# Kernel tuning notes

Measured on AMD Instinct MI355X. Metric: run time of the kernel, lower is better.

The kernel has to match this reference:

```python
import jax, jax.numpy as jnp
import numpy as np

HIDDEN = 2048
N_HEADS = 32
N_KV_HEADS = 4
HEAD_DIM = 128
EPS = 1e-6
ROPE_THETA = 1000000.0
B, S = 1, 2048


def setup_inputs() -> dict:
    key = jax.random.key(0)
    ks = jax.random.split(key, 7)
    scale = 0.02
    return {
        "hidden_states": jax.random.normal(ks[0], (B, S, HIDDEN), jnp.float32),
        "wq": jax.random.normal(ks[1], (HIDDEN, N_HEADS * HEAD_DIM), jnp.float32) * scale,
        "wk": jax.random.normal(ks[2], (HIDDEN, N_KV_HEADS * HEAD_DIM), jnp.float32) * scale,
        "wv": jax.random.normal(ks[3], (HIDDEN, N_KV_HEADS * HEAD_DIM), jnp.float32) * scale,
        "wo": jax.random.normal(ks[4], (N_HEADS * HEAD_DIM, HIDDEN), jnp.float32) * scale,
        "q_norm_w": jnp.ones((HEAD_DIM,), jnp.float32),
        "k_norm_w": jnp.ones((HEAD_DIM,), jnp.float32),
    }


def _rmsnorm(x, w, eps=EPS):
    # RMSNorm over last (head_dim) axis, as in Qwen3MoeRMSNorm applied per-head
    var = jnp.mean(jnp.square(x), axis=-1, keepdims=True)
    return x * jax.lax.rsqrt(var + eps) * w


def _rope_cos_sin(seq_len, dtype):
    inv_freq = 1.0 / (ROPE_THETA ** (jnp.arange(0, HEAD_DIM, 2, dtype=jnp.float32) / HEAD_DIM))
    pos = jnp.arange(seq_len, dtype=jnp.float32)
    freqs = pos[:, None] * inv_freq[None, :]          # [S, dh/2]
    emb = jnp.concatenate([freqs, freqs], axis=-1)    # [S, dh]
    return jnp.cos(emb).astype(dtype), jnp.sin(emb).astype(dtype)


def _rotate_half(x):
    h = x.shape[-1] // 2
    return jnp.concatenate([-x[..., h:], x[..., :h]], axis=-1)


def reference(hidden_states, wq, wk, wv, wo, q_norm_w, k_norm_w):
    b, s, _ = hidden_states.shape
    # QKV projections (bias-free)
    q = (hidden_states @ wq).reshape(b, s, N_HEADS, HEAD_DIM)
    k = (hidden_states @ wk).reshape(b, s, N_KV_HEADS, HEAD_DIM)
    v = (hidden_states @ wv).reshape(b, s, N_KV_HEADS, HEAD_DIM)
    # per-head RMSNorm on Q and K
    q = _rmsnorm(q, q_norm_w)
    k = _rmsnorm(k, k_norm_w)
    # RoPE (prefill, start_pos = 0)
    cos, sin = _rope_cos_sin(s, q.dtype)              # [S, dh]
    cos = cos[None, :, None, :]
    sin = sin[None, :, None, :]
    q = q * cos + _rotate_half(q) * sin
    k = k * cos + _rotate_half(k) * sin
    # GQA: repeat KV heads to match Q heads
    groups = N_HEADS // N_KV_HEADS
    k = jnp.repeat(k, groups, axis=2)                 # [B,S,nH,dh]
    v = jnp.repeat(v, groups, axis=2)
    # causal SDPA
    scaling = HEAD_DIM ** -0.5
    scores = jnp.einsum("bqhd,bkhd->bhqk", q, k) * scaling
    causal = jnp.tril(jnp.ones((s, s), dtype=bool))
    scores = jnp.where(causal[None, None], scores, jnp.finfo(scores.dtype).min)
    probs = jax.nn.softmax(scores, axis=-1)
    attn = jnp.einsum("bhqk,bkhd->bqhd", probs, v)    # [B,S,nH,dh]
    attn = attn.reshape(b, s, N_HEADS * HEAD_DIM)
    return attn @ wo
```

## Files before the change

### kernel.cpp

```cpp
#include <hip/hip_runtime.h>
#include <stdint.h>

typedef unsigned short u16;
typedef __bf16 bf16x8 __attribute__((ext_vector_type(8)));
typedef float f32x4 __attribute__((ext_vector_type(4)));

#define SEQ 2048
#define QKV_N 5120
#define QN 4096

#if __has_builtin(__builtin_amdgcn_exp2f)
#define EXP2F __builtin_amdgcn_exp2f
#else
#define EXP2F exp2f
#endif

#define QSC (0.08838834764831845f * 1.4426950408889634f)
#define MLOG2E 17.312340490667560f

__device__ __forceinline__ u16 f2bf(float f) {
  union { float f; unsigned u; } v; v.f = f;
  unsigned r = v.u + 0x7fffu + ((v.u >> 16) & 1u);
  return (u16)(r >> 16);
}
__device__ __forceinline__ u16 f2bf_fast(float f) {
  union { float f; unsigned u; } v; v.f = f;
  return (u16)((v.u + 0x8000u) >> 16);
}
__device__ __forceinline__ float bf2f(u16 b) {
  union { unsigned u; float f; } v; v.u = ((unsigned)b) << 16;
  return v.f;
}

__device__ __forceinline__ void gl2lds16(const void* g, void* l) {
  __builtin_amdgcn_global_load_lds((const __attribute__((address_space(1))) void*)g,
                                   (__attribute__((address_space(3))) void*)l, 16, 0, 0);
}

__global__ __launch_bounds__(256) void k_convert(const float* __restrict__ src, u16* __restrict__ dst) {
  int i = (blockIdx.x * 256 + threadIdx.x) * 4;
  float4 v = *(const float4*)(src + i);
  ushort4 o;
  o.x = f2bf(v.x); o.y = f2bf(v.y); o.z = f2bf(v.z); o.w = f2bf(v.w);
  *(ushort4*)(dst + i) = o;
}

__global__ __launch_bounds__(256) void k_transpose(const float* __restrict__ src, u16* __restrict__ dst,
                                                   int R, int C) {
  __shared__ float t[32][33];
  int c0 = blockIdx.x * 32, r0 = blockIdx.y * 32;
  int j = threadIdx.x & 31, i0 = threadIdx.x >> 5;
#pragma unroll
  for (int p = 0; p < 4; ++p) {
    int r = i0 + p * 8;
    t[r][j] = src[(size_t)(r0 + r) * C + c0 + j];
  }
  __syncthreads();
#pragma unroll
  for (int p = 0; p < 4; ++p) {
    int r = i0 + p * 8;
    dst[(size_t)(c0 + r) * R + r0 + j] = f2bf(t[j][r]);
  }
}

__global__ __launch_bounds__(256) void k_gemm160(const u16* __restrict__ A, const u16* __restrict__ BT,
                                                 u16* __restrict__ C, int M, int N, int K) {
  __shared__ u16 As[128 * 64];
  __shared__ u16 Bs[160 * 64];
  const int tid = threadIdx.x;
  const int w = tid >> 6, lane = tid & 63, quad = lane >> 4, l15 = lane & 15;
  const int m0 = blockIdx.y * 128, n0 = blockIdx.x * 160;
  const int mw = (w & 1) * 64, nw = (w >> 1) * 80;

  f32x4 acc[4][5];
#pragma unroll
  for (int i = 0; i < 4; ++i)
#pragma unroll
    for (int j = 0; j < 5; ++j) acc[i][j] = {0.f, 0.f, 0.f, 0.f};

  const int nk = K >> 6;
  for (int kt = 0; kt < nk; ++kt) {
    const int k0 = kt << 6;
    __syncthreads();
#pragma unroll
    for (int p = 0; p < 4; ++p) {
      int ci = (w * 4 + p) * 64 + lane;
      int row = ci >> 3, gc = (ci & 7) ^ (row & 7);
      gl2lds16(A + (size_t)(m0 + row) * K + k0 + gc * 8, As + (w * 4 + p) * 512);
    }
#pragma unroll
    for (int p = 0; p < 5; ++p) {
      int ci = (w * 5 + p) * 64 + lane;
      int row = ci >> 3, gc = (ci & 7) ^ (row & 7);
      gl2lds16(BT + (size_t)(n0 + row) * K + k0 + gc * 8, Bs + (w * 5 + p) * 512);
    }
    __syncthreads();
#pragma unroll
    for (int kk = 0; kk < 2; ++kk) {
      bf16x8 a[4], b[5];
#pragma unroll
      for (int mt = 0; mt < 4; ++mt) {
        int row = mw + mt * 16 + l15;
        a[mt] = *(const bf16x8*)(As + row * 64 + (((kk * 4 + quad) ^ (row & 7)) * 8));
      }
#pragma unroll
      for (int nt = 0; nt < 5; ++nt) {
        int row = nw + nt * 16 + l15;
        b[nt] = *(const bf16x8*)(Bs + row * 64 + (((kk * 4 + quad) ^ (row & 7)) * 8));
      }
#pragma unroll
      for (int mt = 0; mt < 4; ++mt)
#pragma unroll
        for (int nt = 0; nt < 5; ++nt)
          acc[mt][nt] = __builtin_amdgcn_mfma_f32_16x16x32_bf16(a[mt], b[nt], acc[mt][nt], 0, 0, 0);
    }
  }
#pragma unroll
  for (int mt = 0; mt < 4; ++mt)
#pragma unroll
    for (int nt = 0; nt < 5; ++nt)
#pragma unroll
      for (int r = 0; r < 4; ++r) {
        int row = m0 + mw + mt * 16 + quad * 4 + r;
        int col = n0 + nw + nt * 16 + l15;
        C[(size_t)row * N + col] = f2bf(acc[mt][nt][r]);
      }
}

__global__ __launch_bounds__(256) void k_gemm_sk(const u16* __restrict__ A, const u16* __restrict__ BT,
                                                 float* __restrict__ C, int M, int N, int K) {
  __shared__ u16 As[128 * 64];
  __shared__ u16 Bs[128 * 64];
  const int tid = threadIdx.x;
  const int w = tid >> 6, lane = tid & 63, quad = lane >> 4, l15 = lane & 15;
  const int m0 = blockIdx.y * 128, n0 = blockIdx.x * 128;
  const int mw = (w & 1) * 64, nw = (w >> 1) * 64;
  const int khalf = K >> 1;
  const int kbase = blockIdx.z * khalf;

  f32x4 acc[4][4];
#pragma unroll
  for (int i = 0; i < 4; ++i)
#pragma unroll
    for (int j = 0; j < 4; ++j) acc[i][j] = {0.f, 0.f, 0.f, 0.f};

  const int nk = khalf >> 6;
  for (int kt = 0; kt < nk; ++kt) {
    const int k0 = kbase + (kt << 6);
    __syncthreads();
#pragma unroll
    for (int p = 0; p < 4; ++p) {
      int ci = (w * 4 + p) * 64 + lane;
      int row = ci >> 3, gc = (ci & 7) ^ (row & 7);
      gl2lds16(A + (size_t)(m0 + row) * K + k0 + gc * 8, As + (w * 4 + p) * 512);
      gl2lds16(BT + (size_t)(n0 + row) * K + k0 + gc * 8, Bs + (w * 4 + p) * 512);
    }
    __syncthreads();
#pragma unroll
    for (int kk = 0; kk < 2; ++kk) {
      bf16x8 a[4], b[4];
#pragma unroll
      for (int mt = 0; mt < 4; ++mt) {
        int row = mw + mt * 16 + l15;
        a[mt] = *(const bf16x8*)(As + row * 64 + (((kk * 4 + quad) ^ (row & 7)) * 8));
      }
#pragma unroll
      for (int nt = 0; nt < 4; ++nt) {
        int row = nw + nt * 16 + l15;
        b[nt] = *(const bf16x8*)(Bs + row * 64 + (((kk * 4 + quad) ^ (row & 7)) * 8));
      }
#pragma unroll
      for (int mt = 0; mt < 4; ++mt)
#pragma unroll
        for (int nt = 0; nt < 4; ++nt)
          acc[mt][nt] = __builtin_amdgcn_mfma_f32_16x16x32_bf16(a[mt], b[nt], acc[mt][nt], 0, 0, 0);
    }
  }
#pragma unroll
  for (int mt = 0; mt < 4; ++mt)
#pragma unroll
    for (int nt = 0; nt < 4; ++nt)
#pragma unroll
      for (int r = 0; r < 4; ++r) {
        int row = m0 + mw + mt * 16 + quad * 4 + r;
        int col = n0 + nw + nt * 16 + l15;
        atomicAdd(&C[(size_t)row * N + col], acc[mt][nt][r]);
      }
}

__global__ __launch_bounds__(256) void k_postproc(const u16* __restrict__ QKV,
                                                  const float* __restrict__ qw, const float* __restrict__ kw,
                                                  u16* __restrict__ qb, u16* __restrict__ kb) {
  int s = blockIdx.x;
  int w = threadIdx.x >> 6, lane = threadIdx.x & 63;
  const u16* row = QKV + (size_t)s * QKV_N;
  float inv_freq = EXP2F(-(float)lane * (19.931568569324174f / 64.0f));
  float fr = (float)s * inv_freq;
  float sn, cs;
  __sincosf(fr, &sn, &cs);
  float qw0 = qw[lane], qw1 = qw[lane + 64];
  float kw0 = kw[lane], kw1 = kw[lane + 64];
  for (int item = w; item < 36; item += 4) {
    bool isq = item < 32;
    int h = isq ? item : item - 32;
    int base = isq ? h * 128 : 4096 + h * 128;
    float x0 = bf2f(row[base + lane]), x1 = bf2f(row[base + 64 + lane]);
    float ss = x0 * x0 + x1 * x1;
#pragma unroll
    for (int off = 1; off < 64; off <<= 1) ss += __shfl_xor(ss, off);
    float rr = rsqrtf(ss * (1.0f / 128.0f) + 1e-6f);
    float n0 = x0 * rr * (isq ? qw0 : kw0), n1 = x1 * rr * (isq ? qw1 : kw1);
    float y0 = n0 * cs - n1 * sn;
    float y1 = n1 * cs + n0 * sn;
    if (isq) {
      size_t o = (size_t)s * QN + h * 128 + lane;
      qb[o] = f2bf(y0 * QSC);
      qb[o + 64] = f2bf(y1 * QSC);
    } else {
      size_t o = ((size_t)h * SEQ + s) * 128 + lane;
      kb[o] = f2bf(y0);
      kb[o + 64] = f2bf(y1);
    }
  }
}

__global__ __launch_bounds__(256) void k_vtrans(const u16* __restrict__ QKV, u16* __restrict__ vt) {
  __shared__ u16 t[32][34];
  int s0 = blockIdx.x * 32, d0 = blockIdx.y * 32, h = blockIdx.z;
  int j = threadIdx.x & 31, i0 = threadIdx.x >> 5;
#pragma unroll
  for (int p = 0; p < 4; ++p) {
    int r = i0 + p * 8;
    t[r][j] = QKV[(size_t)(s0 + r) * QKV_N + 4608 + h * 128 + d0 + j];
  }
  __syncthreads();
#pragma unroll
  for (int p = 0; p < 4; ++p) {
    int r = i0 + p * 8;
    vt[((size_t)h * 128 + d0 + r) * SEQ + s0 + j] = t[j][r];
  }
}

__global__ __launch_bounds__(256, 2) void k_flash(const u16* __restrict__ qb_, const u16* __restrict__ kb,
                                                  const u16* __restrict__ vt, u16* __restrict__ attn) {
  __shared__ u16 Ks[64 * 128];
  __shared__ u16 Vts[128 * 64];
  __shared__ u16 Ps[4][2048];
  const int bx = blockIdx.x;
  const int slot = bx & 255, phase = bx >> 8;
  const int head = slot & 31;
  const int qblk = phase ? (slot >> 5) : 15 - (slot >> 5);
  const int kvh = head >> 3;
  const int q0 = qblk * 128;
  const int tid = threadIdx.x, w = tid >> 6, lane = tid & 63, quad = lane >> 4, l15 = lane & 15;
  const int rowlo0 = q0 + w * 32, rowlo1 = rowlo0 + 16;

  bf16x8 qf[2][4];
#pragma unroll
  for (int mt = 0; mt < 2; ++mt) {
    const u16* qrow = qb_ + (size_t)(rowlo0 + mt * 16 + l15) * QN + head * 128;
#pragma unroll
    for (int ks = 0; ks < 4; ++ks) qf[mt][ks] = *(const bf16x8*)(qrow + ks * 32 + quad * 8);
  }
  f32x4 o[2][8];
#pragma unroll
  for (int mt = 0; mt < 2; ++mt)
#pragma unroll
    for (int i = 0; i < 8; ++i) o[mt][i] = {0.f, 0.f, 0.f, 0.f};
  float lr[2][4] = {{0.f, 0.f, 0.f, 0.f}, {0.f, 0.f, 0.f, 0.f}};

  const u16* kbase = kb + (size_t)kvh * SEQ * 128;
  const u16* vbase = vt + (size_t)kvh * 128 * SEQ;
  u16* pw = Ps[w];

  const int nT = 2 * qblk + 2;
  for (int ti = 0; ti < nT; ++ti) {
    const int t0 = ti * 64;
    __syncthreads();
#pragma unroll
    for (int p = 0; p < 4; ++p) {
      int ci = (w * 4 + p) * 64 + lane;
      {
        int row = ci >> 4, pc = ci & 15, gc = pc ^ (row & 15);
        gl2lds16(kbase + (size_t)(t0 + row) * 128 + gc * 8, Ks + (w * 4 + p) * 512);
      }
      {
        int d = ci >> 3, pc = ci & 7, gc = pc ^ (d & 7);
        gl2lds16(vbase + (size_t)d * SEQ + t0 + gc * 8, Vts + (w * 4 + p) * 512);
      }
    }
    __syncthreads();

    const bool a0 = t0 < rowlo0 + 16;
    const bool a1 = t0 < rowlo1 + 16;
    if (a1) {
      f32x4 sa[2][4];
#pragma unroll
      for (int mt = 0; mt < 2; ++mt)
#pragma unroll
        for (int nt = 0; nt < 4; ++nt) sa[mt][nt] = {0.f, 0.f, 0.f, 0.f};
#pragma unroll
      for (int nt = 0; nt < 4; ++nt) {
        int row = nt * 16 + l15;
#pragma unroll
        for (int ks = 0; ks < 4; ++ks) {
          bf16x8 kf = *(const bf16x8*)(Ks + row * 128 + (((ks * 4 + quad) ^ (row & 15)) * 8));
          if (a0) sa[0][nt] = __builtin_amdgcn_mfma_f32_16x16x32_bf16(qf[0][ks], kf, sa[0][nt], 0, 0, 0);
          sa[1][nt] = __builtin_amdgcn_mfma_f32_16x16x32_bf16(qf[1][ks], kf, sa[1][nt], 0, 0, 0);
        }
      }
#pragma unroll
      for (int mt = 0; mt < 2; ++mt) {
        if (mt == 0 && !a0) continue;
        const int rl = rowlo0 + mt * 16;
        const bool domask = (t0 + 63 > rl);
        u16* pm = pw + mt * 1024;
#pragma unroll
        for (int nt = 0; nt < 4; ++nt)
#pragma unroll
          for (int r = 0; r < 4; ++r) {
            float p = EXP2F(sa[mt][nt][r] - MLOG2E);
            if (domask) {
              int tcol = t0 + nt * 16 + l15;
              int qrow = rl + quad * 4 + r;
              p = (tcol > qrow) ? 0.f : p;
            }
            sa[mt][nt][r] = p;
            pm[(quad * 4 + r) * 64 + ((nt ^ quad) << 4) + l15] = f2bf_fast(p);
          }
#pragma unroll
        for (int r = 0; r < 4; ++r)
          lr[mt][r] += sa[mt][0][r] + sa[mt][1][r] + sa[mt][2][r] + sa[mt][3][r];
      }
      asm volatile("s_waitcnt lgkmcnt(0)" ::: "memory");
#pragma unroll
      for (int ks2 = 0; ks2 < 2; ++ks2) {
        int col = (ks2 * 32 + quad * 8) ^ ((l15 >> 2) << 4);
        bf16x8 pa0, pa1;
        if (a0) pa0 = *(const bf16x8*)(pw + l15 * 64 + col);
        pa1 = *(const bf16x8*)(pw + 1024 + l15 * 64 + col);
#pragma unroll
        for (int nt2 = 0; nt2 < 8; ++nt2) {
          int d = nt2 * 16 + l15;
          bf16x8 vf = *(const bf16x8*)(Vts + d * 64 + (((ks2 * 4 + quad) ^ (d & 7)) * 8));
          if (a0) o[0][nt2] = __builtin_amdgcn_mfma_f32_16x16x32_bf16(pa0, vf, o[0][nt2], 0, 0, 0);
          o[1][nt2] = __builtin_amdgcn_mfma_f32_16x16x32_bf16(pa1, vf, o[1][nt2], 0, 0, 0);
        }
      }
    }
  }
#pragma unroll
  for (int mt = 0; mt < 2; ++mt) {
    float inv[4];
#pragma unroll
    for (int r = 0; r < 4; ++r) {
      float s = lr[mt][r];
      s += __shfl_xor(s, 1);
      s += __shfl_xor(s, 2);
      s += __shfl_xor(s, 4);
      s += __shfl_xor(s, 8);
      inv[r] = 1.0f / s;
    }
#pragma unroll
    for (int nt2 = 0; nt2 < 8; ++nt2)
#pragma unroll
      for (int r = 0; r < 4; ++r) {
        size_t idx = (size_t)(rowlo0 + mt * 16 + quad * 4 + r) * QN + head * 128 + nt2 * 16 + l15;
        attn[idx] = f2bf_fast(o[mt][nt2][r] * inv[r]);
      }
  }
}

extern "C" void kernel_launch(void* const* d_in, const int* in_sizes, int n_in,
                              void* d_out, int out_size, void* d_ws, size_t ws_size,
                              hipStream_t stream) {
  const float* hidden = (const float*)d_in[0];
  const float* wq = (const float*)d_in[1];
  const float* wk = (const float*)d_in[2];
  const float* wv = (const float*)d_in[3];
  const float* wo = (const float*)d_in[4];
  const float* qnw = (const float*)d_in[5];
  const float* knw = (const float*)d_in[6];
  float* out = (float*)d_out;

  char* ws = (char*)d_ws;
  u16* hid_bf = (u16*)(ws);
  u16* WT = (u16*)(ws + 8388608);
  u16* woT = (u16*)(ws + 29360128);
  u16* QKV = (u16*)(ws + 46137344);
  u16* q_bf = (u16*)(ws + 88080384);
  u16* k_bf = (u16*)(ws + 104857600);
  u16* vt = (u16*)(ws + 106954752);
  u16* attn = (u16*)(ws + 109051904);

  hipMemsetAsync(d_out, 0, (size_t)2048 * 2048 * 4, stream);
  k_convert<<<4096, 256, 0, stream>>>(hidden, hid_bf);
  k_transpose<<<dim3(128, 64), 256, 0, stream>>>(wq, WT, 2048, 4096);
  k_transpose<<<dim3(16, 64), 256, 0, stream>>>(wk, WT + (size_t)4096 * 2048, 2048, 512);
  k_transpose<<<dim3(16, 64), 256, 0, stream>>>(wv, WT + (size_t)4608 * 2048, 2048, 512);
  k_transpose<<<dim3(64, 128), 256, 0, stream>>>(wo, woT, 4096, 2048);
  k_gemm160<<<dim3(32, 16), 256, 0, stream>>>(hid_bf, WT, QKV, 2048, 5120, 2048);
  k_postproc<<<2048, 256, 0, stream>>>(QKV, qnw, knw, q_bf, k_bf);
  k_vtrans<<<dim3(64, 4, 4), 256, 0, stream>>>(QKV, vt);
  k_flash<<<512, 256, 0, stream>>>(q_bf, k_bf, vt, attn);
  k_gemm_sk<<<dim3(16, 16, 2), 256, 0, stream>>>(attn, woT, out, 2048, 2048, 4096);
}
```

Before: 340.9 us.

## Double-buffer LDS tiles in GEMMs and flash attention, merge prep and post kernels

The two GEMM kernels and the flash-attention kernel now keep two LDS buffers. The next K-tile is issued with global_load_lds while the current one is consumed, using explicit vmcnt waits and raw barriers. Separately, the convert and four transpose launches are merged into one k_prep kernel, and postproc plus V-transpose are merged into one k_post kernel, cutting launch overhead. Doubling LDS raises shared-memory use, which may lower occupancy, especially in k_flash with its launch bound of two blocks per CU. The hand-tuned vmcnt counts must also match the number of loads issued.

```diff
diff --git a/kernel.cpp b/kernel.cpp
--- a/kernel.cpp
+++ b/kernel.cpp
@@ -18,6 +18,11 @@
 #define QSC (0.08838834764831845f * 1.4426950408889634f)
 #define MLOG2E 17.312340490667560f
 
+#define WAIT_VM(n) asm volatile("s_waitcnt vmcnt(" #n ")" ::: "memory")
+#define WAIT_LGKM asm volatile("s_waitcnt lgkmcnt(0)" ::: "memory")
+#define FENCE asm volatile("" ::: "memory")
+#define BARRIER_RAW do { FENCE; __builtin_amdgcn_s_barrier(); FENCE; } while (0)
+
 __device__ __forceinline__ u16 f2bf(float f) {
   union { float f; unsigned u; } v; v.f = f;
   unsigned r = v.u + 0x7fffu + ((v.u >> 16) & 1u);
@@ -37,18 +42,36 @@
                                    (__attribute__((address_space(3))) void*)l, 16, 0, 0);
 }
 
-__global__ __launch_bounds__(256) void k_convert(const float* __restrict__ src, u16* __restrict__ dst) {
-  int i = (blockIdx.x * 256 + threadIdx.x) * 4;
-  float4 v = *(const float4*)(src + i);
-  ushort4 o;
-  o.x = f2bf(v.x); o.y = f2bf(v.y); o.z = f2bf(v.z); o.w = f2bf(v.w);
-  *(ushort4*)(dst + i) = o;
-}
-
-__global__ __launch_bounds__(256) void k_transpose(const float* __restrict__ src, u16* __restrict__ dst,
-                                                   int R, int C) {
+__global__ __launch_bounds__(256) void k_prep(const float* __restrict__ hidden,
+                                              const float* __restrict__ wq, const float* __restrict__ wk,
+                                              const float* __restrict__ wv, const float* __restrict__ wo,
+                                              u16* __restrict__ hid_bf, u16* __restrict__ WT,
+                                              u16* __restrict__ woT) {
   __shared__ float t[32][33];
-  int c0 = blockIdx.x * 32, r0 = blockIdx.y * 32;
+  int bx = blockIdx.x;
+  if (bx < 4096) {
+    int i = (bx * 256 + threadIdx.x) * 4;
+    float4 v = *(const float4*)(hidden + i);
+    ushort4 o;
+    o.x = f2bf(v.x); o.y = f2bf(v.y); o.z = f2bf(v.z); o.w = f2bf(v.w);
+    *(ushort4*)(hid_bf + i) = o;
+    return;
+  }
+  const float* src; u16* dst; int R, C, cx, cy;
+  if (bx < 4096 + 8192) {
+    int local = bx - 4096; src = wq; dst = WT; R = 2048; C = 4096;
+    cx = local & 127; cy = local >> 7;
+  } else if (bx < 4096 + 8192 + 1024) {
+    int local = bx - (4096 + 8192); src = wk; dst = WT + (size_t)4096 * 2048; R = 2048; C = 512;
+    cx = local & 15; cy = local >> 4;
+  } else if (bx < 4096 + 8192 + 2048) {
+    int local = bx - (4096 + 8192 + 1024); src = wv; dst = WT + (size_t)4608 * 2048; R = 2048; C = 512;
+    cx = local & 15; cy = local >> 4;
+  } else {
+    int local = bx - (4096 + 8192 + 2048); src = wo; dst = woT; R = 4096; C = 2048;
+    cx = local & 63; cy = local >> 6;
+  }
+  int c0 = cx * 32, r0 = cy * 32;
   int j = threadIdx.x & 31, i0 = threadIdx.x >> 5;
 #pragma unroll
   for (int p = 0; p < 4; ++p) {
@@ -65,8 +88,8 @@
 
 __global__ __launch_bounds__(256) void k_gemm160(const u16* __restrict__ A, const u16* __restrict__ BT,
                                                  u16* __restrict__ C, int M, int N, int K) {
-  __shared__ u16 As[128 * 64];
-  __shared__ u16 Bs[160 * 64];
+  __shared__ u16 As[2][128 * 64];
+  __shared__ u16 Bs[2][160 * 64];
   const int tid = threadIdx.x;
   const int w = tid >> 6, lane = tid & 63, quad = lane >> 4, l15 = lane & 15;
   const int m0 = blockIdx.y * 128, n0 = blockIdx.x * 160;
@@ -78,35 +101,48 @@
 #pragma unroll
     for (int j = 0; j < 5; ++j) acc[i][j] = {0.f, 0.f, 0.f, 0.f};
 
-  const int nk = K >> 6;
-  for (int kt = 0; kt < nk; ++kt) {
+  auto stage = [&](int kt, int buf) {
     const int k0 = kt << 6;
-    __syncthreads();
 #pragma unroll
     for (int p = 0; p < 4; ++p) {
       int ci = (w * 4 + p) * 64 + lane;
       int row = ci >> 3, gc = (ci & 7) ^ (row & 7);
-      gl2lds16(A + (size_t)(m0 + row) * K + k0 + gc * 8, As + (w * 4 + p) * 512);
+      gl2lds16(A + (size_t)(m0 + row) * K + k0 + gc * 8, &As[buf][(w * 4 + p) * 512]);
     }
 #pragma unroll
     for (int p = 0; p < 5; ++p) {
       int ci = (w * 5 + p) * 64 + lane;
       int row = ci >> 3, gc = (ci & 7) ^ (row & 7);
-      gl2lds16(BT + (size_t)(n0 + row) * K + k0 + gc * 8, Bs + (w * 5 + p) * 512);
-    }
-    __syncthreads();
+      gl2lds16(BT + (size_t)(n0 + row) * K + k0 + gc * 8, &Bs[buf][(w * 5 + p) * 512]);
+    }
+  };
+
+  const int nk = K >> 6;
+  stage(0, 0);
+  for (int kt = 0; kt < nk; ++kt) {
+    WAIT_LGKM;
+    BARRIER_RAW;
+    if (kt + 1 < nk) {
+      stage(kt + 1, (kt + 1) & 1);
+      WAIT_VM(9);
+    } else {
+      WAIT_VM(0);
+    }
+    BARRIER_RAW;
+    const u16* Ac = As[kt & 1];
+    const u16* Bc = Bs[kt & 1];
 #pragma unroll
     for (int kk = 0; kk < 2; ++kk) {
       bf16x8 a[4], b[5];
 #pragma unroll
       for (int mt = 0; mt < 4; ++mt) {
         int row = mw + mt * 16 + l15;
-        a[mt] = *(const bf16x8*)(As + row * 64 + (((kk * 4 + quad) ^ (row & 7)) * 8));
+        a[mt] = *(const bf16x8*)(Ac + row * 64 + (((kk * 4 + quad) ^ (row & 7)) * 8));
       }
 #pragma unroll
       for (int nt = 0; nt < 5; ++nt) {
         int row = nw + nt * 16 + l15;
-        b[nt] = *(const bf16x8*)(Bs + row * 64 + (((kk * 4 + quad) ^ (row & 7)) * 8));
+        b[nt] = *(const bf16x8*)(Bc + row * 64 + (((kk * 4 + quad) ^ (row & 7)) * 8));
       }
 #pragma unroll
       for (int mt = 0; mt < 4; ++mt)
@@ -129,8 +165,8 @@
 
 __global__ __launch_bounds__(256) void k_gemm_sk(const u16* __restrict__ A, const u16* __restrict__ BT,
                                                  float* __restrict__ C, int M, int N, int K) {
-  __shared__ u16 As[128 * 64];
-  __shared__ u16 Bs[128 * 64];
+  __shared__ u16 As[2][128 * 64];
+  __shared__ u16 Bs[2][128 * 64];
   const int tid = threadIdx.x;
   const int w = tid >> 6, lane = tid & 63, quad = lane >> 4, l15 = lane & 15;
   const int m0 = blockIdx.y * 128, n0 = blockIdx.x * 128;
@@ -144,30 +180,43 @@
 #pragma unroll
     for (int j = 0; j < 4; ++j) acc[i][j] = {0.f, 0.f, 0.f, 0.f};
 
-  const int nk = khalf >> 6;
-  for (int kt = 0; kt < nk; ++kt) {
+  auto stage = [&](int kt, int buf) {
     const int k0 = kbase + (kt << 6);
-    __syncthreads();
 #pragma unroll
     for (int p = 0; p < 4; ++p) {
       int ci = (w * 4 + p) * 64 + lane;
       int row = ci >> 3, gc = (ci & 7) ^ (row & 7);
-      gl2lds16(A + (size_t)(m0 + row) * K + k0 + gc * 8, As + (w * 4 + p) * 512);
-      gl2lds16(BT + (size_t)(n0 + row) * K + k0 + gc * 8, Bs + (w * 4 + p) * 512);
-    }
-    __syncthreads();
+      gl2lds16(A + (size_t)(m0 + row) * K + k0 + gc * 8, &As[buf][(w * 4 + p) * 512]);
+      gl2lds16(BT + (size_t)(n0 + row) * K + k0 + gc * 8, &Bs[buf][(w * 4 + p) * 512]);
+    }
+  };
+
+  const int nk = khalf >> 6;
+  stage(0, 0);
+  for (int kt = 0; kt < nk; ++kt) {
+    WAIT_LGKM;
+    BARRIER_RAW;
+    if (kt + 1 < nk) {
+      stage(kt + 1, (kt + 1) & 1);
+      WAIT_VM(8);
+    } else {
+      WAIT_VM(0);
+    }
+    BARRIER_RAW;
+    const u16* Ac = As[kt & 1];
+    const u16* Bc = Bs[kt & 1];
 #pragma unroll
     for (int kk = 0; kk < 2; ++kk) {
       bf16x8 a[4], b[4];
 #pragma unroll
       for (int mt = 0; mt < 4; ++mt) {
         int row = mw + mt * 16 + l15;
-        a[mt] = *(const bf16x8*)(As + row * 64 + (((kk * 4 + quad) ^ (row & 7)) * 8));
+        a[mt] = *(const bf16x8*)(Ac + row * 64 + (((kk * 4 + quad) ^ (row & 7)) * 8));
       }
 #pragma unroll
       for (int nt = 0; nt < 4; ++nt) {
         int row = nw + nt * 16 + l15;
-        b[nt] = *(const bf16x8*)(Bs + row * 64 + (((kk * 4 + quad) ^ (row & 7)) * 8));
+        b[nt] = *(const bf16x8*)(Bc + row * 64 + (((kk * 4 + quad) ^ (row & 7)) * 8));
       }
 #pragma unroll
       for (int mt = 0; mt < 4; ++mt)
@@ -188,45 +237,48 @@
       }
 }
 
-__global__ __launch_bounds__(256) void k_postproc(const u16* __restrict__ QKV,
-                                                  const float* __restrict__ qw, const float* __restrict__ kw,
-                                                  u16* __restrict__ qb, u16* __restrict__ kb) {
-  int s = blockIdx.x;
-  int w = threadIdx.x >> 6, lane = threadIdx.x & 63;
-  const u16* row = QKV + (size_t)s * QKV_N;
-  float inv_freq = EXP2F(-(float)lane * (19.931568569324174f / 64.0f));
-  float fr = (float)s * inv_freq;
-  float sn, cs;
-  __sincosf(fr, &sn, &cs);
-  float qw0 = qw[lane], qw1 = qw[lane + 64];
-  float kw0 = kw[lane], kw1 = kw[lane + 64];
-  for (int item = w; item < 36; item += 4) {
-    bool isq = item < 32;
-    int h = isq ? item : item - 32;
-    int base = isq ? h * 128 : 4096 + h * 128;
-    float x0 = bf2f(row[base + lane]), x1 = bf2f(row[base + 64 + lane]);
-    float ss = x0 * x0 + x1 * x1;
-#pragma unroll
-    for (int off = 1; off < 64; off <<= 1) ss += __shfl_xor(ss, off);
-    float rr = rsqrtf(ss * (1.0f / 128.0f) + 1e-6f);
-    float n0 = x0 * rr * (isq ? qw0 : kw0), n1 = x1 * rr * (isq ? qw1 : kw1);
-    float y0 = n0 * cs - n1 * sn;
-    float y1 = n1 * cs + n0 * sn;
-    if (isq) {
-      size_t o = (size_t)s * QN + h * 128 + lane;
-      qb[o] = f2bf(y0 * QSC);
-      qb[o + 64] = f2bf(y1 * QSC);
-    } else {
-      size_t o = ((size_t)h * SEQ + s) * 128 + lane;
-      kb[o] = f2bf(y0);
-      kb[o + 64] = f2bf(y1);
-    }
-  }
-}
-
-__global__ __launch_bounds__(256) void k_vtrans(const u16* __restrict__ QKV, u16* __restrict__ vt) {
+__global__ __launch_bounds__(256) void k_post(const u16* __restrict__ QKV,
+                                              const float* __restrict__ qw, const float* __restrict__ kw,
+                                              u16* __restrict__ qb, u16* __restrict__ kb,
+                                              u16* __restrict__ vt) {
   __shared__ u16 t[32][34];
-  int s0 = blockIdx.x * 32, d0 = blockIdx.y * 32, h = blockIdx.z;
+  int bx = blockIdx.x;
+  if (bx < 2048) {
+    int s = bx;
+    int w = threadIdx.x >> 6, lane = threadIdx.x & 63;
+    const u16* row = QKV + (size_t)s * QKV_N;
+    float inv_freq = EXP2F(-(float)lane * (19.931568569324174f / 64.0f));
+    float fr = (float)s * inv_freq;
+    float sn, cs;
+    __sincosf(fr, &sn, &cs);
+    float qw0 = qw[lane], qw1 = qw[lane + 64];
+    float kw0 = kw[lane], kw1 = kw[lane + 64];
+    for (int item = w; item < 36; item += 4) {
+      bool isq = item < 32;
+      int h = isq ? item : item - 32;
+      int base = isq ? h * 128 : 4096 + h * 128;
+      float x0 = bf2f(row[base + lane]), x1 = bf2f(row[base + 64 + lane]);
+      float ss = x0 * x0 + x1 * x1;
+#pragma unroll
+      for (int off = 1; off < 64; off <<= 1) ss += __shfl_xor(ss, off);
+      float rr = rsqrtf(ss * (1.0f / 128.0f) + 1e-6f);
+      float n0 = x0 * rr * (isq ? qw0 : kw0), n1 = x1 * rr * (isq ? qw1 : kw1);
+      float y0 = n0 * cs - n1 * sn;
+      float y1 = n1 * cs + n0 * sn;
+      if (isq) {
+        size_t o = (size_t)s * QN + h * 128 + lane;
+        qb[o] = f2bf(y0 * QSC);
+        qb[o + 64] = f2bf(y1 * QSC);
+      } else {
+        size_t o = ((size_t)h * SEQ + s) * 128 + lane;
+        kb[o] = f2bf(y0);
+        kb[o + 64] = f2bf(y1);
+      }
+    }
+    return;
+  }
+  int local = bx - 2048;
+  int s0 = (local & 63) * 32, d0 = ((local >> 6) & 3) * 32, h = local >> 8;
   int j = threadIdx.x & 31, i0 = threadIdx.x >> 5;
 #pragma unroll
   for (int p = 0; p < 4; ++p) {
@@ -243,8 +295,8 @@
 
 __global__ __launch_bounds__(256, 2) void k_flash(const u16* __restrict__ qb_, const u16* __restrict__ kb,
                                                   const u16* __restrict__ vt, u16* __restrict__ attn) {
-  __shared__ u16 Ks[64 * 128];
-  __shared__ u16 Vts[128 * 64];
+  __shared__ u16 Ks[2][64 * 128];
+  __shared__ u16 Vts[2][128 * 64];
   __shared__ u16 Ps[4][2048];
   const int bx = blockIdx.x;
   const int slot = bx & 255, phase = bx >> 8;
@@ -273,23 +325,37 @@
   const u16* vbase = vt + (size_t)kvh * 128 * SEQ;
   u16* pw = Ps[w];
 
-  const int nT = 2 * qblk + 2;
-  for (int ti = 0; ti < nT; ++ti) {
+  auto stage = [&](int ti, int buf) {
     const int t0 = ti * 64;
-    __syncthreads();
 #pragma unroll
     for (int p = 0; p < 4; ++p) {
       int ci = (w * 4 + p) * 64 + lane;
       {
-        int row = ci >> 4, pc = ci & 15, gc = pc ^ (row & 15);
-        gl2lds16(kbase + (size_t)(t0 + row) * 128 + gc * 8, Ks + (w * 4 + p) * 512);
+        int row = ci >> 4, gc = (ci & 15) ^ (row & 15);
+        gl2lds16(kbase + (size_t)(t0 + row) * 128 + gc * 8, &Ks[buf][(w * 4 + p) * 512]);
       }
       {
-        int d = ci >> 3, pc = ci & 7, gc = pc ^ (d & 7);
-        gl2lds16(vbase + (size_t)d * SEQ + t0 + gc * 8, Vts + (w * 4 + p) * 512);
-      }
-    }
-    __syncthreads();
+        int d = ci >> 3, gc = (ci & 7) ^ (d & 7);
+        gl2lds16(vbase + (size_t)d * SEQ + t0 + gc * 8, &Vts[buf][(w * 4 + p) * 512]);
+      }
+    }
+  };
+
+  const int nT = 2 * qblk + 2;
+  stage(0, 0);
+  for (int ti = 0; ti < nT; ++ti) {
+    const int t0 = ti * 64;
+    WAIT_LGKM;
+    BARRIER_RAW;
+    if (ti + 1 < nT) {
+      stage(ti + 1, (ti + 1) & 1);
+      WAIT_VM(8);
+    } else {
+      WAIT_VM(0);
+    }
+    BARRIER_RAW;
+    const u16* Kc = Ks[ti & 1];
+    const u16* Vc = Vts[ti & 1];
 
     const bool a0 = t0 < rowlo0 + 16;
     const bool a1 = t0 < rowlo1 + 16;
@@ -304,7 +370,7 @@
         int row = nt * 16 + l15;
 #pragma unroll
         for (int ks = 0; ks < 4; ++ks) {
-          bf16x8 kf = *(const bf16x8*)(Ks + row * 128 + (((ks * 4 + quad) ^ (row & 15)) * 8));
+          bf16x8 kf = *(const bf16x8*)(Kc + row * 128 + (((ks * 4 + quad) ^ (row & 15)) * 8));
           if (a0) sa[0][nt] = __builtin_amdgcn_mfma_f32_16x16x32_bf16(qf[0][ks], kf, sa[0][nt], 0, 0, 0);
           sa[1][nt] = __builtin_amdgcn_mfma_f32_16x16x32_bf16(qf[1][ks], kf, sa[1][nt], 0, 0, 0);
         }
@@ -332,7 +398,7 @@
         for (int r = 0; r < 4; ++r)
           lr[mt][r] += sa[mt][0][r] + sa[mt][1][r] + sa[mt][2][r] + sa[mt][3][r];
       }
-      asm volatile("s_waitcnt lgkmcnt(0)" ::: "memory");
+      WAIT_LGKM;
 #pragma unroll
       for (int ks2 = 0; ks2 < 2; ++ks2) {
         int col = (ks2 * 32 + quad * 8) ^ ((l15 >> 2) << 4);
@@ -342,7 +408,7 @@
 #pragma unroll
         for (int nt2 = 0; nt2 < 8; ++nt2) {
           int d = nt2 * 16 + l15;
-          bf16x8 vf = *(const bf16x8*)(Vts + d * 64 + (((ks2 * 4 + quad) ^ (d & 7)) * 8));
+          bf16x8 vf = *(const bf16x8*)(Vc + d * 64 + (((ks2 * 4 + quad) ^ (d & 7)) * 8));
           if (a0) o[0][nt2] = __builtin_amdgcn_mfma_f32_16x16x32_bf16(pa0, vf, o[0][nt2], 0, 0, 0);
           o[1][nt2] = __builtin_amdgcn_mfma_f32_16x16x32_bf16(pa1, vf, o[1][nt2], 0, 0, 0);
         }
@@ -394,14 +460,9 @@
   u16* attn = (u16*)(ws + 109051904);
 
   hipMemsetAsync(d_out, 0, (size_t)2048 * 2048 * 4, stream);
-  k_convert<<<4096, 256, 0, stream>>>(hidden, hid_bf);
-  k_transpose<<<dim3(128, 64), 256, 0, stream>>>(wq, WT, 2048, 4096);
-  k_transpose<<<dim3(16, 64), 256, 0, stream>>>(wk, WT + (size_t)4096 * 2048, 2048, 512);
-  k_transpose<<<dim3(16, 64), 256, 0, stream>>>(wv, WT + (size_t)4608 * 2048, 2048, 512);
-  k_transpose<<<dim3(64, 128), 256, 0, stream>>>(wo, woT, 4096, 2048);
+  k_prep<<<22528, 256, 0, stream>>>(hidden, wq, wk, wv, wo, hid_bf, WT, woT);
   k_gemm160<<<dim3(32, 16), 256, 0, stream>>>(hid_bf, WT, QKV, 2048, 5120, 2048);
-  k_postproc<<<2048, 256, 0, stream>>>(QKV, qnw, knw, q_bf, k_bf);
-  k_vtrans<<<dim3(64, 4, 4), 256, 0, stream>>>(QKV, vt);
+  k_post<<<3072, 256, 0, stream>>>(QKV, qnw, knw, q_bf, k_bf, vt);
   k_flash<<<512, 256, 0, stream>>>(q_bf, k_bf, vt, attn);
   k_gemm_sk<<<dim3(16, 16, 2), 256, 0, stream>>>(attn, woT, out, 2048, 2048, 4096);
 }
```

After: 317.5 us. -6.9%, faster.
